# Kernel optimization log

Hardware: AMD Instinct MI355X
Metric: run time of the kernel (lower is better)

The kernel has to match this reference:

```python
import jax, jax.numpy as jnp
import numpy as np

T, B, H = 2048, 8, 1024


def setup_inputs() -> dict:
    key = jax.random.key(0)
    ks = jax.random.split(key, 4)
    scale = 1.0 / np.sqrt(H)
    x = jax.random.normal(ks[0], (T, B, H), dtype=jnp.float32)
    W_q = jax.random.normal(ks[1], (H, H), dtype=jnp.float32) * scale
    b_q = jnp.zeros((H,), dtype=jnp.float32)
    beta_raw = jax.random.normal(ks[2], (H,), dtype=jnp.float32)
    W_fc = jax.random.normal(ks[3], (H, H), dtype=jnp.float32) * scale
    b_fc = jnp.zeros((H,), dtype=jnp.float32)
    return {"x": x, "W_q": W_q, "b_q": b_q, "beta_raw": beta_raw,
            "W_fc": W_fc, "b_fc": b_fc}


def reference(x, W_q, b_q, beta_raw, W_fc, b_fc):
    # Per-neuron learned leak in (0,1)
    beta = jax.nn.sigmoid(beta_raw)  # (H,)
    # Input (q) projection: (T,B,H) @ (H,H)^T
    q = jnp.einsum('tbh,oh->tbo', x, W_q) + b_q  # (T,B,H)
    # Leaky integration m_t = beta * m_{t-1} + q_t as an associative scan over T
    a = jnp.broadcast_to(beta, q.shape)  # (T,B,H)

    def combine(c1, c2):
        a1, m1 = c1
        a2, m2 = c2
        return (a1 * a2, a2 * m1 + m2)

    _, m = jax.lax.associative_scan(combine, (a, q), axis=0)  # (T,B,H)
    # Linear + ReLU
    h = jnp.einsum('tbh,oh->tbo', m, W_fc) + b_fc
    return jax.nn.relu(h)
```

## Files before the change

### kernel.cpp

```cpp
#include <hip/hip_runtime.h>
#include <stdint.h>

typedef unsigned short u16;
typedef __bf16 bf16x8 __attribute__((ext_vector_type(8)));
typedef float f32x4 __attribute__((ext_vector_type(4)));

__device__ __forceinline__ u16 f2bf(float f) {
  union { float f; uint32_t u; } x; x.f = f;
  uint32_t u = x.u;
  u += 0x7fffu + ((u >> 16) & 1u);
  return (u16)(u >> 16);
}
__device__ __forceinline__ float bf2f(uint32_t lo16) {
  union { uint32_t u; float f; } x; x.u = lo16 << 16; return x.f;
}

__device__ __forceinline__ void async_load16(const u16* g, u16* l) {
  __builtin_amdgcn_global_load_lds(
      (const __attribute__((address_space(1))) void*)g,
      (__attribute__((address_space(3))) void*)l,
      16, 0, 0);
}

__global__ __launch_bounds__(256) void prep_all(const float* __restrict__ x,
                                                const float* __restrict__ Wq,
                                                const float* __restrict__ Wfc,
                                                const float* __restrict__ braw,
                                                u16* __restrict__ xb,
                                                u16* __restrict__ wqb,
                                                u16* __restrict__ wfcb,
                                                float* __restrict__ beta) {
  int gid = blockIdx.x * 256 + threadIdx.x;
  if (gid < 1024) beta[gid] = 1.0f / (1.0f + expf(-braw[gid]));
  if (gid < 131072) {
    const int HH = 1024 * 1024;
    int i = gid * 16;
    const float* src = (i < HH) ? (Wq + i) : (Wfc + (i - HH));
    u16* dst = (i < HH) ? (wqb + i) : (wfcb + (i - HH));
#pragma unroll
    for (int c = 0; c < 4; c++) {
      float4 v = *(const float4*)(src + c * 4);
      ushort4 o = {f2bf(v.x), f2bf(v.y), f2bf(v.z), f2bf(v.w)};
      *(ushort4*)(dst + c * 4) = o;
    }
  }
  {
    int i = gid * 8;
    float4 a = *(const float4*)(x + i);
    float4 b = *(const float4*)(x + i + 4);
    ushort4 o0 = {f2bf(a.x), f2bf(a.y), f2bf(a.z), f2bf(a.w)};
    ushort4 o1 = {f2bf(b.x), f2bf(b.y), f2bf(b.z), f2bf(b.w)};
    *(ushort4*)(xb + i) = o0;
    *(ushort4*)(xb + i + 4) = o1;
  }
}

template <int RELU, int OUTBF>
__global__ __launch_bounds__(256) void gemm_bt(const u16* __restrict__ A,
                                               const u16* __restrict__ B,
                                               const float* __restrict__ bias,
                                               void* __restrict__ Cout,
                                               int M, int N, int K) {
  __shared__ u16 As[128 * 64];
  __shared__ u16 Bs[128 * 64];

  const int tid  = threadIdx.x;
  const int lane = tid & 63;

  const int L  = blockIdx.x;
  const int xc = L & 7;
  const int k8 = L >> 3;
  const int tile_n = (k8 & 7) * 128;
  const int tile_m = ((xc << 4) | (k8 >> 3)) * 128;

  const int wm = ((tid >> 7) & 1) * 64;
  const int wn = ((tid >> 6) & 1) * 64;

  const int srow   = tid >> 3;
  const int schunk = (tid & 7) ^ ((tid >> 3) & 7);
  u16* ldsA = &As[((tid >> 6) * 8) * 64];
  u16* ldsB = &Bs[((tid >> 6) * 8) * 64];

  const u16* gA = A + (size_t)(tile_m + srow) * K + schunk * 8;
  const u16* gB = B + (size_t)(tile_n + srow) * K + schunk * 8;

  f32x4 acc[4][4];
#pragma unroll
  for (int i = 0; i < 4; i++)
#pragma unroll
    for (int j = 0; j < 4; j++) acc[i][j] = (f32x4){0.f, 0.f, 0.f, 0.f};

  const int lrow = lane & 15;
  const int kq   = lane >> 4;

  for (int k0 = 0; k0 < K; k0 += 64) {
    __syncthreads();
#pragma unroll
    for (int i = 0; i < 4; i++) {
      async_load16(gA + (size_t)(i * 32) * K + k0, ldsA + i * 32 * 64);
      async_load16(gB + (size_t)(i * 32) * K + k0, ldsB + i * 32 * 64);
    }
    __builtin_amdgcn_s_waitcnt(0);
    __syncthreads();

#pragma unroll
    for (int js = 0; js < 2; js++) {
      const int cc = ((kq + 4 * js) ^ (lane & 7)) << 3;
      bf16x8 a[4], b[4];
#pragma unroll
      for (int i = 0; i < 4; i++)
        a[i] = *(const bf16x8*)&As[(wm + i * 16 + lrow) * 64 + cc];
#pragma unroll
      for (int j = 0; j < 4; j++)
        b[j] = *(const bf16x8*)&Bs[(wn + j * 16 + lrow) * 64 + cc];
#pragma unroll
      for (int i = 0; i < 4; i++)
#pragma unroll
        for (int j = 0; j < 4; j++)
          acc[i][j] = __builtin_amdgcn_mfma_f32_16x16x32_bf16(a[i], b[j], acc[i][j], 0, 0, 0);
    }
  }

  const int crow = (lane >> 4) << 2;
  const int ccol = lane & 15;
#pragma unroll
  for (int i = 0; i < 4; i++) {
#pragma unroll
    for (int j = 0; j < 4; j++) {
      const int gm = tile_m + wm + i * 16 + crow;
      const int gn = tile_n + wn + j * 16 + ccol;
      const float bv = bias[gn];
#pragma unroll
      for (int r = 0; r < 4; r++) {
        float v = acc[i][j][r] + bv;
        if (RELU) v = fmaxf(v, 0.f);
        if (OUTBF) ((u16*)Cout)[(size_t)(gm + r) * N + gn] = f2bf(v);
        else       ((float*)Cout)[(size_t)(gm + r) * N + gn] = v;
      }
    }
  }
}

#define NCH 8192
#define SEG 32
#define NSEG 64

__global__ __launch_bounds__(256) void scan_carry(const uint2* __restrict__ qb,
                                                  float* __restrict__ carry,
                                                  const float* __restrict__ beta_arr) {
  int tid = blockIdx.x * 256 + threadIdx.x;
  int seg = tid >> 11;
  int cq  = tid & 2047;
  int h0  = (cq * 4) & 1023;
  float b0 = beta_arr[h0], b1 = beta_arr[h0 + 1], b2 = beta_arr[h0 + 2], b3 = beta_arr[h0 + 3];
  const uint2* p = qb + (size_t)seg * SEG * 2048 + cq;
  float m0 = 0.f, m1 = 0.f, m2 = 0.f, m3 = 0.f;
#pragma unroll 8
  for (int t = 0; t < SEG; t++) {
    uint2 v = p[(size_t)t * 2048];
    m0 = fmaf(b0, m0, bf2f(v.x & 0xffffu));
    m1 = fmaf(b1, m1, bf2f(v.x >> 16));
    m2 = fmaf(b2, m2, bf2f(v.y & 0xffffu));
    m3 = fmaf(b3, m3, bf2f(v.y >> 16));
  }
  *(float4*)&carry[(size_t)seg * NCH + cq * 4] = make_float4(m0, m1, m2, m3);
}

__global__ __launch_bounds__(256) void scan_fuse(const uint2* __restrict__ qb,
                                                 const float4* __restrict__ carry4,
                                                 const float* __restrict__ beta_arr,
                                                 uint2* __restrict__ mb) {
  const int tid = blockIdx.x * 256 + threadIdx.x;
  const int seg = tid >> 11;
  const int cq  = tid & 2047;
  const int h0  = (cq * 4) & 1023;
  const float b0 = beta_arr[h0], b1 = beta_arr[h0 + 1];
  const float b2 = beta_arr[h0 + 2], b3 = beta_arr[h0 + 3];
  float s0 = b0, s1 = b1, s2 = b2, s3 = b3;
#pragma unroll
  for (int i = 0; i < 5; i++) { s0 *= s0; s1 *= s1; s2 *= s2; s3 *= s3; }
  float m0 = 0.f, m1 = 0.f, m2 = 0.f, m3 = 0.f;
  const float4* cp = carry4 + cq;
  for (int s = 0; s < seg; s++) {
    float4 c = cp[(size_t)s * 2048];
    m0 = fmaf(s0, m0, c.x); m1 = fmaf(s1, m1, c.y);
    m2 = fmaf(s2, m2, c.z); m3 = fmaf(s3, m3, c.w);
  }
  const uint2* p = qb + (size_t)seg * SEG * 2048 + cq;
  uint2* o = mb + (size_t)seg * SEG * 2048 + cq;
#pragma unroll 8
  for (int t = 0; t < SEG; t++) {
    uint2 v = p[(size_t)t * 2048];
    m0 = fmaf(b0, m0, bf2f(v.x & 0xffffu));
    m1 = fmaf(b1, m1, bf2f(v.x >> 16));
    m2 = fmaf(b2, m2, bf2f(v.y & 0xffffu));
    m3 = fmaf(b3, m3, bf2f(v.y >> 16));
    uint2 w;
    w.x = (uint32_t)f2bf(m0) | ((uint32_t)f2bf(m1) << 16);
    w.y = (uint32_t)f2bf(m2) | ((uint32_t)f2bf(m3) << 16);
    o[(size_t)t * 2048] = w;
  }
}

extern "C" void kernel_launch(void* const* d_in, const int* in_sizes, int n_in,
                              void* d_out, int out_size, void* d_ws, size_t ws_size,
                              hipStream_t stream) {
  const float* x        = (const float*)d_in[0];
  const float* W_q      = (const float*)d_in[1];
  const float* b_q      = (const float*)d_in[2];
  const float* beta_raw = (const float*)d_in[3];
  const float* W_fc     = (const float*)d_in[4];
  const float* b_fc     = (const float*)d_in[5];

  const int H = 1024;
  const int M = 2048 * 8;
  const size_t MH = (size_t)M * H;

  char* ws = (char*)d_ws;
  u16* x_bf    = (u16*)ws;  ws += MH * 2;
  u16* q_bf    = (u16*)ws;  ws += MH * 2;
  u16* m_bf    = (u16*)ws;  ws += MH * 2;
  u16* wq_bf   = (u16*)ws;  ws += (size_t)H * H * 2;
  u16* wfc_bf  = (u16*)ws;  ws += (size_t)H * H * 2;
  float* beta  = (float*)ws; ws += 4096;
  float* carry = (float*)ws; ws += (size_t)NSEG * NCH * 4;

  prep_all<<<(int)(MH / 8 / 256), 256, 0, stream>>>(x, W_q, W_fc, beta_raw,
                                                    x_bf, wq_bf, wfc_bf, beta);

  gemm_bt<0, 1><<<1024, 256, 0, stream>>>(x_bf, wq_bf, b_q, q_bf, M, H, H);

  scan_carry<<<NSEG * (NCH / 4) / 256, 256, 0, stream>>>((const uint2*)q_bf, carry, beta);
  scan_fuse<<<NSEG * (NCH / 4) / 256, 256, 0, stream>>>((const uint2*)q_bf,
                                                        (const float4*)carry, beta,
                                                        (uint2*)m_bf);

  gemm_bt<1, 0><<<1024, 256, 0, stream>>>(m_bf, wfc_bf, b_fc, d_out, M, H, H);
}
```

Measured before the change: 254.6 us.

## Replace GEMM with 256x256-tile, 4-stage async-pipelined MFMA kernel

Rewrites the bf16 GEMM to use 256x256 output tiles with 512 threads and a 4-slot LDS ring buffer fed by async global-to-LDS loads three k-steps ahead. Partial vmcnt waits and a single barrier per k-step replace the load-wait-sync-compute loop. MFMA bursts run at raised wave priority. This aims to hide memory latency and improve operand reuse, at the cost of fewer blocks (one wave of 256) and heavy LDS and register use.

```diff
diff --git a/kernel.cpp b/kernel.cpp
--- a/kernel.cpp
+++ b/kernel.cpp
@@ -56,79 +56,104 @@
 }
 
 template <int RELU, int OUTBF>
-__global__ __launch_bounds__(256) void gemm_bt(const u16* __restrict__ A,
-                                               const u16* __restrict__ B,
-                                               const float* __restrict__ bias,
-                                               void* __restrict__ Cout,
-                                               int M, int N, int K) {
-  __shared__ u16 As[128 * 64];
-  __shared__ u16 Bs[128 * 64];
+__global__ __launch_bounds__(512, 2) void gemm256(const u16* __restrict__ A,
+                                                  const u16* __restrict__ B,
+                                                  const float* __restrict__ bias,
+                                                  void* __restrict__ Cout,
+                                                  int M, int N, int K) {
+  __shared__ u16 lds[4][2][256 * 32];
 
   const int tid  = threadIdx.x;
   const int lane = tid & 63;
-
-  const int L  = blockIdx.x;
-  const int xc = L & 7;
-  const int k8 = L >> 3;
-  const int tile_n = (k8 & 7) * 128;
-  const int tile_m = ((xc << 4) | (k8 >> 3)) * 128;
-
-  const int wm = ((tid >> 7) & 1) * 64;
-  const int wn = ((tid >> 6) & 1) * 64;
-
-  const int srow   = tid >> 3;
-  const int schunk = (tid & 7) ^ ((tid >> 3) & 7);
-  u16* ldsA = &As[((tid >> 6) * 8) * 64];
-  u16* ldsB = &Bs[((tid >> 6) * 8) * 64];
-
+  const int wid  = tid >> 6;
+  const int wr   = (wid >> 2) * 128;
+  const int wc   = (wid & 3) * 64;
+
+  const int bid    = blockIdx.x;
+  const int tile_m = (bid >> 2) * 256;
+  const int tile_n = (bid & 3) * 256;
+
+  const int srow    = tid >> 2;
+  const int schunk  = (tid & 3) ^ ((srow >> 1) & 3);
   const u16* gA = A + (size_t)(tile_m + srow) * K + schunk * 8;
   const u16* gB = B + (size_t)(tile_n + srow) * K + schunk * 8;
-
-  f32x4 acc[4][4];
-#pragma unroll
-  for (int i = 0; i < 4; i++)
+  const size_t half_stride = (size_t)128 * K;
+
+#define STAGE(slot, kt)                                                   \
+  do {                                                                    \
+    const size_t k0 = (size_t)(kt) * 32;                                  \
+    async_load16(gA + k0,               &lds[slot][0][wid * 512]);        \
+    async_load16(gA + k0 + half_stride, &lds[slot][0][4096 + wid * 512]); \
+    async_load16(gB + k0,               &lds[slot][1][wid * 512]);        \
+    async_load16(gB + k0 + half_stride, &lds[slot][1][4096 + wid * 512]); \
+  } while (0)
+
+  f32x4 acc[8][4];
+#pragma unroll
+  for (int i = 0; i < 8; i++)
 #pragma unroll
     for (int j = 0; j < 4; j++) acc[i][j] = (f32x4){0.f, 0.f, 0.f, 0.f};
 
   const int lrow = lane & 15;
   const int kq   = lane >> 4;
-
-  for (int k0 = 0; k0 < K; k0 += 64) {
-    __syncthreads();
-#pragma unroll
-    for (int i = 0; i < 4; i++) {
-      async_load16(gA + (size_t)(i * 32) * K + k0, ldsA + i * 32 * 64);
-      async_load16(gB + (size_t)(i * 32) * K + k0, ldsB + i * 32 * 64);
+  const int kc   = (lrow >> 1) & 3;
+  const int coff = ((kq ^ kc) << 3);
+
+  const int NKT = K >> 5;
+
+  STAGE(0, 0);
+  if (NKT > 1) STAGE(1, 1);
+  if (NKT > 2) STAGE(2, 2);
+  if (NKT > 2)      asm volatile("s_waitcnt vmcnt(8)" ::: "memory");
+  else if (NKT > 1) asm volatile("s_waitcnt vmcnt(4)" ::: "memory");
+  else              asm volatile("s_waitcnt vmcnt(0)" ::: "memory");
+  __builtin_amdgcn_s_barrier();
+
+  for (int kt = 0; kt < NKT; ++kt) {
+    const int slot = kt & 3;
+    const u16* As = &lds[slot][0][0];
+    const u16* Bs = &lds[slot][1][0];
+
+    bf16x8 a[8], b[4];
+#pragma unroll
+    for (int i = 0; i < 8; i++)
+      a[i] = *(const bf16x8*)&As[(wr + i * 16 + lrow) * 32 + coff];
+#pragma unroll
+    for (int j = 0; j < 4; j++)
+      b[j] = *(const bf16x8*)&Bs[(wc + j * 16 + lrow) * 32 + coff];
+
+    if (kt + 3 < NKT) STAGE((kt + 3) & 3, kt + 3);
+
+    __builtin_amdgcn_s_setprio(1);
+#pragma unroll
+    for (int i = 0; i < 8; i++)
+#pragma unroll
+      for (int j = 0; j < 4; j++)
+        acc[i][j] = __builtin_amdgcn_mfma_f32_16x16x32_bf16(a[i], b[j], acc[i][j], 0, 0, 0);
+    __builtin_amdgcn_s_setprio(0);
+
+    const int ahead = NKT - 1 - kt;
+    if (ahead >= 3) {
+      asm volatile("s_waitcnt vmcnt(8)" ::: "memory");
+      __builtin_amdgcn_s_barrier();
+    } else if (ahead == 2) {
+      asm volatile("s_waitcnt vmcnt(4)" ::: "memory");
+      __builtin_amdgcn_s_barrier();
+    } else if (ahead == 1) {
+      asm volatile("s_waitcnt vmcnt(0)" ::: "memory");
+      __builtin_amdgcn_s_barrier();
     }
-    __builtin_amdgcn_s_waitcnt(0);
-    __syncthreads();
-
-#pragma unroll
-    for (int js = 0; js < 2; js++) {
-      const int cc = ((kq + 4 * js) ^ (lane & 7)) << 3;
-      bf16x8 a[4], b[4];
-#pragma unroll
-      for (int i = 0; i < 4; i++)
-        a[i] = *(const bf16x8*)&As[(wm + i * 16 + lrow) * 64 + cc];
-#pragma unroll
-      for (int j = 0; j < 4; j++)
-        b[j] = *(const bf16x8*)&Bs[(wn + j * 16 + lrow) * 64 + cc];
-#pragma unroll
-      for (int i = 0; i < 4; i++)
-#pragma unroll
-        for (int j = 0; j < 4; j++)
-          acc[i][j] = __builtin_amdgcn_mfma_f32_16x16x32_bf16(a[i], b[j], acc[i][j], 0, 0, 0);
-    }
-  }
+  }
+#undef STAGE
 
   const int crow = (lane >> 4) << 2;
   const int ccol = lane & 15;
 #pragma unroll
-  for (int i = 0; i < 4; i++) {
+  for (int i = 0; i < 8; i++) {
 #pragma unroll
     for (int j = 0; j < 4; j++) {
-      const int gm = tile_m + wm + i * 16 + crow;
-      const int gn = tile_n + wn + j * 16 + ccol;
+      const int gm = tile_m + wr + i * 16 + crow;
+      const int gn = tile_n + wc + j * 16 + ccol;
       const float bv = bias[gn];
 #pragma unroll
       for (int r = 0; r < 4; r++) {
@@ -228,12 +253,12 @@
   prep_all<<<(int)(MH / 8 / 256), 256, 0, stream>>>(x, W_q, W_fc, beta_raw,
                                                     x_bf, wq_bf, wfc_bf, beta);
 
-  gemm_bt<0, 1><<<1024, 256, 0, stream>>>(x_bf, wq_bf, b_q, q_bf, M, H, H);
+  gemm256<0, 1><<<256, 512, 0, stream>>>(x_bf, wq_bf, b_q, q_bf, M, H, H);
 
   scan_carry<<<NSEG * (NCH / 4) / 256, 256, 0, stream>>>((const uint2*)q_bf, carry, beta);
   scan_fuse<<<NSEG * (NCH / 4) / 256, 256, 0, stream>>>((const uint2*)q_bf,
                                                         (const float4*)carry, beta,
                                                         (uint2*)m_bf);
 
-  gemm_bt<1, 0><<<1024, 256, 0, stream>>>(m_bf, wfc_bf, b_fc, d_out, M, H, H);
-}
+  gemm256<1, 0><<<256, 512, 0, stream>>>(m_bf, wfc_bf, b_fc, d_out, M, H, H);
+}
```

After: 240.1 us. 5.7% less time.
